# Kernel tuning notes

Hardware: AMD Instinct MI355X
Metric: run time of the kernel (lower is better)

Reference implementation:

```python
import jax, jax.numpy as jnp
import numpy as np

N = 100000
E = 1200000
D = 64
EPS = 1e-15
ATANH_CLIP = 1.0 - 1e-7


def _logmap0(x, c):
    # Poincare ball logmap at origin: artanh(sqrt(c)||x||) * x / (sqrt(c)||x||)
    sqrt_c = jnp.sqrt(c)
    norm = jnp.maximum(jnp.linalg.norm(x, axis=-1, keepdims=True), EPS)
    arg = jnp.minimum(sqrt_c * norm, ATANH_CLIP)
    return jnp.arctanh(arg) * x / (sqrt_c * norm)


def _expmap0(u, c):
    # Poincare ball expmap at origin: tanh(sqrt(c)||u||) * u / (sqrt(c)||u||)
    sqrt_c = jnp.sqrt(c)
    norm = jnp.maximum(jnp.linalg.norm(u, axis=-1, keepdims=True), EPS)
    return jnp.tanh(sqrt_c * norm) * u / (sqrt_c * norm)


def setup_inputs() -> dict:
    key = jax.random.key(0)
    ks = jax.random.split(key, 8)
    src = jax.random.randint(ks[0], (E,), 0, N)
    dst = jax.random.randint(ks[1], (E,), 0, N)
    # scale embeddings so points lie inside the unit Poincare ball
    emb = jax.random.normal(ks[2], (N, D), dtype=jnp.float32) * 0.01
    W1 = jax.random.normal(ks[3], (D, D), dtype=jnp.float32) * 0.05
    b1 = jax.random.normal(ks[4], (D,), dtype=jnp.float32) * 0.01
    W2 = jax.random.normal(ks[5], (D, D), dtype=jnp.float32) * 0.05
    b2 = jax.random.normal(ks[6], (D,), dtype=jnp.float32) * 0.01
    curvature = -jnp.ones((1,), dtype=jnp.float32)
    return {"src": src, "dst": dst, "emb": emb, "W1": W1, "b1": b1,
            "W2": W2, "b2": b2, "curvature": curvature}


def reference(src, dst, emb, W1, b1, W2, b2, curvature):
    c = jnp.abs(curvature)[0]
    # in-degree for DGL-style mean (zero-degree nodes get 0)
    deg = jax.ops.segment_sum(jnp.ones((E,), dtype=emb.dtype), dst, num_segments=N)
    inv_deg = jnp.where(deg > 0, 1.0 / jnp.maximum(deg, 1.0), 0.0)[:, None]

    x = emb
    for W, b in ((W1, b1), (W2, b2)):
        tangent = _logmap0(x, c)                         # [N, D]
        h = tangent @ W.T + b                            # [N, D]
        neigh = jax.ops.segment_sum(h[src], dst, num_segments=N) * inv_deg  # scatter-mean
        x = _expmap0(neigh, c)
    return x
```

## Files before the change

kernel.cpp:

```cpp
#include <hip/hip_runtime.h>
#include <math.h>

#define DIM 64
#define EPSF 1e-15f

#define BW_SHIFT 8
#define BW (1 << BW_SHIFT)
#define CAP_SHIFT 12
#define CAP (1 << CAP_SHIFT)

typedef __attribute__((ext_vector_type(8))) short short8;
typedef __attribute__((ext_vector_type(4))) float floatx4;
typedef __attribute__((ext_vector_type(2))) float floatx2;
typedef __attribute__((ext_vector_type(4))) unsigned int uintx4;

__device__ __forceinline__ float group16_sum(float x) {
#pragma unroll
    for (int off = 1; off <= 8; off <<= 1)
        x += __shfl_xor(x, off, 64);
    return x;
}
__device__ __forceinline__ float group8_sum(float x) {
#pragma unroll
    for (int off = 1; off <= 4; off <<= 1)
        x += __shfl_xor(x, off, 64);
    return x;
}
__device__ __forceinline__ unsigned int f2bf(float x) {
    unsigned int u = __float_as_uint(x);
    u += 0x7fffu + ((u >> 16) & 1u);
    return u >> 16;
}
__device__ __forceinline__ float bflo(unsigned int u) { return __uint_as_float(u << 16); }
__device__ __forceinline__ float bfhi(unsigned int u) { return __uint_as_float(u & 0xFFFF0000u); }

__global__ void prep_kernel(const float* __restrict__ W1, const float* __restrict__ W2,
                            unsigned short* __restrict__ Wbf1, unsigned short* __restrict__ Wbf2,
                            unsigned short* __restrict__ zrowb, int* __restrict__ cursorB, int NB) {
    int i = blockIdx.x * 256 + threadIdx.x;
    if (i < DIM * DIM) {
        Wbf1[i] = (unsigned short)f2bf(W1[i]);
        Wbf2[i] = (unsigned short)f2bf(W2[i]);
    }
    if (i < NB) cursorB[i] = i << CAP_SHIFT;
    if (blockIdx.x == 0 && threadIdx.x < 64) zrowb[threadIdx.x] = 0;
}

__global__ __launch_bounds__(256) void partition_kernel(
    const int* __restrict__ src, const int* __restrict__ dst,
    int* __restrict__ cursorB, unsigned int* __restrict__ pairBuf, int E, int NB)
{
    __shared__ int hist[512], gbase[512], lcur[512];
    int tid = threadIdx.x;
    for (int t = tid; t < NB; t += 256) { hist[t] = 0; lcur[t] = 0; }
    __syncthreads();
    int base = blockIdx.x * 4096;
    unsigned int packed[16]; int bkt[16];
#pragma unroll
    for (int i = 0; i < 16; ++i) {
        int e = base + i * 256 + tid;
        if (e < E) {
            int s = src[e], d = dst[e];
            bkt[i] = d >> BW_SHIFT;
            packed[i] = ((unsigned int)(d & (BW - 1)) << 17) | (unsigned int)s;
            atomicAdd(&hist[bkt[i]], 1);
        } else bkt[i] = -1;
    }
    __syncthreads();
    for (int t = tid; t < NB; t += 256)
        gbase[t] = hist[t] ? atomicAdd(&cursorB[t], hist[t]) : 0;
    __syncthreads();
#pragma unroll
    for (int i = 0; i < 16; ++i) {
        if (bkt[i] >= 0) {
            int rank = atomicAdd(&lcur[bkt[i]], 1);
            int p = gbase[bkt[i]] + rank;
            if (p < ((bkt[i] + 1) << CAP_SHIFT)) pairBuf[p] = packed[i];
        }
    }
}

union SharedU {
    struct {
        int edges[CAP];
        int stage[CAP];
        int hist[BW], cur[BW], tmp[BW];
    } s;
    unsigned int atile[4][16 * 36];
};

__global__ __launch_bounds__(256, 4) void sort_and_gemm_kernel(
    const unsigned int* __restrict__ pairBuf, const int* __restrict__ cursorB,
    int* __restrict__ rowS, int* __restrict__ rowE, int* __restrict__ col,
    const float* __restrict__ in, const unsigned short* __restrict__ Wbf,
    const float* __restrict__ bias, const float* __restrict__ curv,
    unsigned short* __restrict__ outb, int N, int NB)
{
    __shared__ SharedU u;
    if ((int)blockIdx.x < NB) {
        const int b = blockIdx.x, t = threadIdx.x;
        const int base = b << CAP_SHIFT;
        int cnt = cursorB[b] - base;
        if (cnt > CAP) cnt = CAP;
        for (int i = t; i < cnt; i += 256) u.s.edges[i] = (int)pairBuf[base + i];
        u.s.hist[t] = 0;
        __syncthreads();
        for (int i = t; i < cnt; i += 256) atomicAdd(&u.s.hist[u.s.edges[i] >> 17], 1);
        __syncthreads();
        int hv = u.s.hist[t];
        u.s.tmp[t] = hv; __syncthreads();
        for (int off = 1; off < 256; off <<= 1) {
            int x = (t >= off) ? u.s.tmp[t - off] : 0; __syncthreads();
            u.s.tmp[t] += x; __syncthreads();
        }
        int excl = u.s.tmp[t] - hv;
        int node = (b << BW_SHIFT) + t;
        if (node < N) { rowS[node] = base + excl; rowE[node] = base + excl + hv; }
        u.s.cur[t] = excl;
        __syncthreads();
        for (int i = t; i < cnt; i += 256) {
            int v = u.s.edges[i];
            int pos = atomicAdd(&u.s.cur[v >> 17], 1);
            u.s.stage[pos] = v & 0x1FFFF;
        }
        __syncthreads();
        for (int i = t; i < cnt; i += 256) col[base + i] = u.s.stage[i];
    } else {
        const int bid = blockIdx.x - NB;
        const int gemmWaves = (gridDim.x - NB) << 2;
        const float sc = sqrtf(fabsf(curv[0]));
        const float CLIPF = 1.0f - 1e-7f;
        const int lane = threadIdx.x & 63;
        const int wid  = threadIdx.x >> 6;
        const int q = lane >> 4, r = lane & 15;
        const int numBatches = (N + 15) >> 4;
        const float4* in4 = (const float4*)in;

        short8 bfrag[4][2];
#pragma unroll
        for (int nt = 0; nt < 4; ++nt)
#pragma unroll
            for (int ks = 0; ks < 2; ++ks)
                bfrag[nt][ks] = *(const short8*)(Wbf + (nt * 16 + r) * 64 + ks * 32 + q * 8);

        float biasv[4];
#pragma unroll
        for (int nt = 0; nt < 4; ++nt) biasv[nt] = bias[nt * 16 + r];

        for (int batch = (bid << 2) + wid; batch < numBatches; batch += gemmWaves) {
            const int base = batch << 4;
#pragma unroll
            for (int it = 0; it < 4; ++it) {
                int m = it * 4 + q;
                int node = base + m;
                float4 v = make_float4(0.f, 0.f, 0.f, 0.f);
                if (node < N) v = in4[(size_t)node * 16 + r];
                float ss = group16_sum(v.x * v.x + v.y * v.y + v.z * v.z + v.w * v.w);
                float nrm = fmaxf(sqrtf(ss), EPSF);
                float a = fminf(sc * nrm, CLIPF);
                float g = atanhf(a) / (sc * nrm);
                unsigned int lo = f2bf(v.x * g) | (f2bf(v.y * g) << 16);
                unsigned int hi = f2bf(v.z * g) | (f2bf(v.w * g) << 16);
                *(uint2*)&u.atile[wid][m * 36 + r * 2] = make_uint2(lo, hi);
            }
            floatx4 accm[4];
#pragma unroll
            for (int nt = 0; nt < 4; ++nt) accm[nt] = (floatx4){0.f, 0.f, 0.f, 0.f};
#pragma unroll
            for (int ks = 0; ks < 2; ++ks) {
                uintx4 ua = *(const uintx4*)&u.atile[wid][r * 36 + q * 4 + ks * 16];
                short8 af = __builtin_bit_cast(short8, ua);
#pragma unroll
                for (int nt = 0; nt < 4; ++nt)
                    accm[nt] = __builtin_amdgcn_mfma_f32_16x16x32_bf16(af, bfrag[nt][ks], accm[nt], 0, 0, 0);
            }
#pragma unroll
            for (int nt = 0; nt < 4; ++nt)
#pragma unroll
                for (int reg = 0; reg < 4; ++reg) {
                    int node = base + q * 4 + reg;
                    if (node < N)
                        outb[(size_t)node * 64 + nt * 16 + r] =
                            (unsigned short)f2bf(accm[nt][reg] + biasv[nt]);
                }
        }
    }
}

__device__ __forceinline__ void gather_rows_bf16(
    const char* __restrict__ hb, const int* __restrict__ col,
    int start, int end, int dmax, long long zoff, int g, int r, int colMax,
    floatx2 acc2[4])
{
    const int roff = r << 4;
    for (int b = 0; (b << 3) < dmax; ++b) {
        int pos = start + (b << 3) + r;
        int cv = col[min(pos, colMax)];
        int sent = (pos < end) ? cv : -1;
        int lim = dmax - (b << 3); if (lim > 8) lim = 8;
        if (lim == 8) {
            long long o[8];
#pragma unroll
            for (int i = 0; i < 8; ++i) {
                int s = __shfl(sent, (g << 3) + i, 64);
                o[i] = (s < 0) ? zoff : ((long long)s << 7);
            }
#pragma unroll
            for (int i = 0; i < 8; ++i) {
                uint4 uu = *(const uint4*)(hb + o[i] + roff);
                acc2[0] += (floatx2){bflo(uu.x), bfhi(uu.x)};
                acc2[1] += (floatx2){bflo(uu.y), bfhi(uu.y)};
                acc2[2] += (floatx2){bflo(uu.z), bfhi(uu.z)};
                acc2[3] += (floatx2){bflo(uu.w), bfhi(uu.w)};
            }
        } else {
            for (int i = 0; i < lim; ++i) {
                int s = __shfl(sent, (g << 3) + i, 64);
                long long o = (s < 0) ? zoff : ((long long)s << 7);
                uint4 uu = *(const uint4*)(hb + o + roff);
                acc2[0] += (floatx2){bflo(uu.x), bfhi(uu.x)};
                acc2[1] += (floatx2){bflo(uu.y), bfhi(uu.y)};
                acc2[2] += (floatx2){bflo(uu.z), bfhi(uu.z)};
                acc2[3] += (floatx2){bflo(uu.w), bfhi(uu.w)};
            }
        }
    }
}

__global__ __launch_bounds__(256, 4) void gather_gemm_mfma(
    const unsigned short* __restrict__ h, const int* __restrict__ rowS,
    const int* __restrict__ rowE, const int* __restrict__ col,
    const unsigned short* __restrict__ Wbf, const float* __restrict__ bias,
    unsigned short* __restrict__ outb, long long zoff, int N, int colMax)
{
    __shared__ unsigned int AtileU[4][16 * 36];
    const int lane = threadIdx.x & 63;
    const int wid  = threadIdx.x >> 6;
    const int q = lane >> 4, r = lane & 15;
    const int g8 = lane >> 3, r8 = lane & 7;
    const int wavesTotal = (gridDim.x * blockDim.x) >> 6;
    const int numBatches = (N + 15) >> 4;
    const char* hb = (const char*)h;

    short8 bfrag[4][2];
#pragma unroll
    for (int nt = 0; nt < 4; ++nt)
#pragma unroll
        for (int ks = 0; ks < 2; ++ks)
            bfrag[nt][ks] = *(const short8*)(Wbf + (nt * 16 + r) * 64 + ks * 32 + q * 8);

    float biasv[4];
#pragma unroll
    for (int nt = 0; nt < 4; ++nt) biasv[nt] = bias[nt * 16 + r];

    for (int batch = (blockIdx.x << 2) + wid; batch < numBatches; batch += wavesTotal) {
        const int base = batch << 4;
#pragma unroll
        for (int it = 0; it < 2; ++it) {
            int m = it * 8 + g8;
            int node = base + m;
            int start = 0, end = 0;
            if (node < N) { start = rowS[node]; end = rowE[node]; }
            int deg = end - start;
            int dmax = max(deg, __shfl_xor(deg, 8, 64));
            dmax = max(dmax, __shfl_xor(dmax, 16, 64));
            dmax = max(dmax, __shfl_xor(dmax, 32, 64));
            floatx2 acc2[4] = {{0.f,0.f},{0.f,0.f},{0.f,0.f},{0.f,0.f}};
            gather_rows_bf16(hb, col, start, end, dmax, zoff, g8, r8, colMax, acc2);
            float inv = (deg > 0) ? 1.f / (float)deg : 0.f;
            unsigned int u0 = f2bf(acc2[0].x * inv) | (f2bf(acc2[0].y * inv) << 16);
            unsigned int u1 = f2bf(acc2[1].x * inv) | (f2bf(acc2[1].y * inv) << 16);
            unsigned int u2 = f2bf(acc2[2].x * inv) | (f2bf(acc2[2].y * inv) << 16);
            unsigned int u3 = f2bf(acc2[3].x * inv) | (f2bf(acc2[3].y * inv) << 16);
            *(uint4*)&AtileU[wid][m * 36 + r8 * 4] = make_uint4(u0, u1, u2, u3);
        }
        floatx4 accm[4];
#pragma unroll
        for (int nt = 0; nt < 4; ++nt) accm[nt] = (floatx4){0.f, 0.f, 0.f, 0.f};
#pragma unroll
        for (int ks = 0; ks < 2; ++ks) {
            uintx4 ua = *(const uintx4*)&AtileU[wid][r * 36 + q * 4 + ks * 16];
            short8 af = __builtin_bit_cast(short8, ua);
#pragma unroll
            for (int nt = 0; nt < 4; ++nt)
                accm[nt] = __builtin_amdgcn_mfma_f32_16x16x32_bf16(af, bfrag[nt][ks], accm[nt], 0, 0, 0);
        }
#pragma unroll
        for (int nt = 0; nt < 4; ++nt)
#pragma unroll
            for (int reg = 0; reg < 4; ++reg) {
                int node = base + q * 4 + reg;
                if (node < N)
                    outb[(size_t)node * 64 + nt * 16 + r] =
                        (unsigned short)f2bf(accm[nt][reg] + biasv[nt]);
            }
    }
}

__global__ __launch_bounds__(256, 6) void gather_expmap8(
    const unsigned short* __restrict__ h, const int* __restrict__ rowS,
    const int* __restrict__ rowE, const int* __restrict__ col,
    const float* __restrict__ curv, float* __restrict__ out,
    long long zoff, int N, int colMax)
{
    const float sc = sqrtf(fabsf(curv[0]));
    const int lane = threadIdx.x & 63;
    const int wid  = threadIdx.x >> 6;
    const int g8 = lane >> 3, r8 = lane & 7;
    const int wavesTotal = (gridDim.x * blockDim.x) >> 6;
    const int numBatches = (N + 7) >> 3;
    const char* hb = (const char*)h;
    float4* out4 = (float4*)out;

    for (int batch = (blockIdx.x << 2) + wid; batch < numBatches; batch += wavesTotal) {
        int node = (batch << 3) + g8;
        int start = 0, end = 0;
        if (node < N) { start = rowS[node]; end = rowE[node]; }
        int deg = end - start;
        int dmax = max(deg, __shfl_xor(deg, 8, 64));
        dmax = max(dmax, __shfl_xor(dmax, 16, 64));
        dmax = max(dmax, __shfl_xor(dmax, 32, 64));
        floatx2 acc2[4] = {{0.f,0.f},{0.f,0.f},{0.f,0.f},{0.f,0.f}};
        gather_rows_bf16(hb, col, start, end, dmax, zoff, g8, r8, colMax, acc2);
        float inv = (deg > 0) ? 1.f / (float)deg : 0.f;
        float v[8], ss = 0.f;
#pragma unroll
        for (int j = 0; j < 4; ++j) {
            v[2*j]   = acc2[j].x * inv;
            v[2*j+1] = acc2[j].y * inv;
            ss += v[2*j] * v[2*j] + v[2*j+1] * v[2*j+1];
        }
        ss = group8_sum(ss);
        float nrm = fmaxf(sqrtf(ss), EPSF);
        float a = sc * nrm;
        float f = tanhf(a) / a;
        if (node < N) {
            out4[(size_t)node * 16 + r8 * 2]     = make_float4(v[0] * f, v[1] * f, v[2] * f, v[3] * f);
            out4[(size_t)node * 16 + r8 * 2 + 1] = make_float4(v[4] * f, v[5] * f, v[6] * f, v[7] * f);
        }
    }
}

extern "C" void kernel_launch(void* const* d_in, const int* in_sizes, int n_in,
                              void* d_out, int out_size, void* d_ws, size_t ws_size,
                              hipStream_t stream)
{
    const int*   src  = (const int*)d_in[0];
    const int*   dst  = (const int*)d_in[1];
    const float* emb  = (const float*)d_in[2];
    const float* W1   = (const float*)d_in[3];
    const float* b1   = (const float*)d_in[4];
    const float* W2   = (const float*)d_in[5];
    const float* b2   = (const float*)d_in[6];
    const float* curv = (const float*)d_in[7];
    float*       out  = (float*)d_out;

    const int E = in_sizes[0];
    const int N = in_sizes[2] / DIM;
    const int NB = (N + BW - 1) >> BW_SHIFT;
    const size_t bucketSlots = (size_t)NB << CAP_SHIFT;
    const int colMax = (int)bucketSlots - 1;

    char* ws = (char*)d_ws;
    auto align256 = [](size_t x) { return (x + 255) & ~(size_t)255; };
    size_t off = 0;
    int* cursorB            = (int*)(ws + off);            off += align256(512 * 4);
    int* rowS               = (int*)(ws + off);            off += align256((size_t)N * 4);
    int* rowE               = (int*)(ws + off);            off += align256((size_t)N * 4);
    unsigned int* pairBuf   = (unsigned int*)(ws + off);   off += align256(bucketSlots * 4);
    int* col                = (int*)(ws + off);            off += align256(bucketSlots * 4);
    unsigned short* Wbf1    = (unsigned short*)(ws + off); off += align256((size_t)DIM * DIM * 2);
    unsigned short* Wbf2    = (unsigned short*)(ws + off); off += align256((size_t)DIM * DIM * 2);
    unsigned short* zrowb   = (unsigned short*)(ws + off); off += align256(DIM * 2);
    unsigned short* h1b     = (unsigned short*)(ws + off); off += align256((size_t)N * DIM * 2);
    unsigned short* h2b     = (unsigned short*)(ws + off); off += align256((size_t)N * DIM * 2);

    const long long zoff_h1 = (long long)((char*)zrowb - (char*)h1b);
    const long long zoff_h2 = (long long)((char*)zrowb - (char*)h2b);

    const int chunkBlocks  = (E + 4095) / 4096;
    const int numBatches16 = (N + 15) / 16;
    const int blocks16     = (numBatches16 + 3) / 4;
    const int numBatches8  = (N + 7) / 8;
    const int blocks8      = (numBatches8 + 3) / 4;

    prep_kernel<<<(DIM * DIM + 255) / 256, 256, 0, stream>>>(W1, W2, Wbf1, Wbf2,
                                                             zrowb, cursorB, NB);
    partition_kernel<<<chunkBlocks, 256, 0, stream>>>(src, dst, cursorB, pairBuf, E, NB);
    sort_and_gemm_kernel<<<NB + blocks16, 256, 0, stream>>>(
        pairBuf, cursorB, rowS, rowE, col, emb, Wbf1, b1, curv, h1b, N, NB);
    gather_gemm_mfma<<<blocks16, 256, 0, stream>>>(h1b, rowS, rowE, col, Wbf2, b2, h2b,
                                                   zoff_h1, N, colMax);
    gather_expmap8<<<blocks8, 256, 0, stream>>>(h2b, rowS, rowE, col, curv, out,
                                                zoff_h2, N, colMax);
}
```

Before: 188.3 us.

## Route neighbor row gathers through global_load_lds DMA into shared staging buffers

Replaces the per-lane register gathers of bf16 neighbor rows with global_load_lds 16-byte DMA transfers into a per-wave LDS staging buffer, then reads the data back from LDS to accumulate. The aim is to cut VGPR pressure and issue overhead on the irregular gather. The trade-off is extra LDS traffic and full vmcnt and lgkmcnt waits on every 8-edge block, which serialise load and consume. The expmap kernel's launch-bounds occupancy hint drops from 6 to 4 to make room for the added 32 KB of LDS per block.

```diff
diff --git a/kernel.cpp b/kernel.cpp
--- a/kernel.cpp
+++ b/kernel.cpp
@@ -33,6 +33,14 @@
 }
 __device__ __forceinline__ float bflo(unsigned int u) { return __uint_as_float(u << 16); }
 __device__ __forceinline__ float bfhi(unsigned int u) { return __uint_as_float(u & 0xFFFF0000u); }
+
+__device__ __forceinline__ void dma16(const void* g, void* l) {
+    __builtin_amdgcn_global_load_lds(
+        (const __attribute__((address_space(1))) unsigned int*)g,
+        (__attribute__((address_space(3))) unsigned int*)l, 16, 0, 0);
+}
+#define WAIT_VM0()   __builtin_amdgcn_s_waitcnt(0x0F70)
+#define WAIT_LGKM0() __builtin_amdgcn_s_waitcnt(0xC07F)
 
 __global__ void prep_kernel(const float* __restrict__ W1, const float* __restrict__ W2,
                             unsigned short* __restrict__ Wbf1, unsigned short* __restrict__ Wbf2,
@@ -187,42 +195,33 @@
     }
 }
 
-__device__ __forceinline__ void gather_rows_bf16(
+__device__ __forceinline__ void gather_rows_dma(
     const char* __restrict__ hb, const int* __restrict__ col,
-    int start, int end, int dmax, long long zoff, int g, int r, int colMax,
-    floatx2 acc2[4])
+    int start, int end, int dmax, long long zoff, int g, int r, int lane,
+    int colMax, uint4* wbuf, floatx2 acc2[4])
 {
     const int roff = r << 4;
-    for (int b = 0; (b << 3) < dmax; ++b) {
-        int pos = start + (b << 3) + r;
+    const char* zptr = hb + zoff;
+    char* wb = (char*)wbuf;
+    for (int sblk = 0; sblk < dmax; sblk += 8) {
+        int pos = start + sblk + r;
         int cv = col[min(pos, colMax)];
         int sent = (pos < end) ? cv : -1;
-        int lim = dmax - (b << 3); if (lim > 8) lim = 8;
-        if (lim == 8) {
-            long long o[8];
-#pragma unroll
-            for (int i = 0; i < 8; ++i) {
-                int s = __shfl(sent, (g << 3) + i, 64);
-                o[i] = (s < 0) ? zoff : ((long long)s << 7);
-            }
-#pragma unroll
-            for (int i = 0; i < 8; ++i) {
-                uint4 uu = *(const uint4*)(hb + o[i] + roff);
-                acc2[0] += (floatx2){bflo(uu.x), bfhi(uu.x)};
-                acc2[1] += (floatx2){bflo(uu.y), bfhi(uu.y)};
-                acc2[2] += (floatx2){bflo(uu.z), bfhi(uu.z)};
-                acc2[3] += (floatx2){bflo(uu.w), bfhi(uu.w)};
-            }
-        } else {
-            for (int i = 0; i < lim; ++i) {
-                int s = __shfl(sent, (g << 3) + i, 64);
-                long long o = (s < 0) ? zoff : ((long long)s << 7);
-                uint4 uu = *(const uint4*)(hb + o + roff);
-                acc2[0] += (floatx2){bflo(uu.x), bfhi(uu.x)};
-                acc2[1] += (floatx2){bflo(uu.y), bfhi(uu.y)};
-                acc2[2] += (floatx2){bflo(uu.z), bfhi(uu.z)};
-                acc2[3] += (floatx2){bflo(uu.w), bfhi(uu.w)};
-            }
+        WAIT_LGKM0();
+#pragma unroll
+        for (int i = 0; i < 8; ++i) {
+            int s = __shfl(sent, (g << 3) + i, 64);
+            const char* gp = (s < 0) ? zptr : (hb + ((long long)s << 7));
+            dma16(gp + roff, (void*)(wb + i * 1024));
+        }
+        WAIT_VM0();
+#pragma unroll
+        for (int i = 0; i < 8; ++i) {
+            uint4 uu = *(const uint4*)(wb + i * 1024 + lane * 16);
+            acc2[0] += (floatx2){bflo(uu.x), bfhi(uu.x)};
+            acc2[1] += (floatx2){bflo(uu.y), bfhi(uu.y)};
+            acc2[2] += (floatx2){bflo(uu.z), bfhi(uu.z)};
+            acc2[3] += (floatx2){bflo(uu.w), bfhi(uu.w)};
         }
     }
 }
@@ -234,6 +233,7 @@
     unsigned short* __restrict__ outb, long long zoff, int N, int colMax)
 {
     __shared__ unsigned int AtileU[4][16 * 36];
+    __shared__ uint4 gbuf[4][512];
     const int lane = threadIdx.x & 63;
     const int wid  = threadIdx.x >> 6;
     const int q = lane >> 4, r = lane & 15;
@@ -241,6 +241,7 @@
     const int wavesTotal = (gridDim.x * blockDim.x) >> 6;
     const int numBatches = (N + 15) >> 4;
     const char* hb = (const char*)h;
+    uint4* wbuf = gbuf[wid];
 
     short8 bfrag[4][2];
 #pragma unroll
@@ -266,7 +267,7 @@
             dmax = max(dmax, __shfl_xor(dmax, 16, 64));
             dmax = max(dmax, __shfl_xor(dmax, 32, 64));
             floatx2 acc2[4] = {{0.f,0.f},{0.f,0.f},{0.f,0.f},{0.f,0.f}};
-            gather_rows_bf16(hb, col, start, end, dmax, zoff, g8, r8, colMax, acc2);
+            gather_rows_dma(hb, col, start, end, dmax, zoff, g8, r8, lane, colMax, wbuf, acc2);
             float inv = (deg > 0) ? 1.f / (float)deg : 0.f;
             unsigned int u0 = f2bf(acc2[0].x * inv) | (f2bf(acc2[0].y * inv) << 16);
             unsigned int u1 = f2bf(acc2[1].x * inv) | (f2bf(acc2[1].y * inv) << 16);
@@ -297,12 +298,13 @@
     }
 }
 
-__global__ __launch_bounds__(256, 6) void gather_expmap8(
+__global__ __launch_bounds__(256, 4) void gather_expmap8(
     const unsigned short* __restrict__ h, const int* __restrict__ rowS,
     const int* __restrict__ rowE, const int* __restrict__ col,
     const float* __restrict__ curv, float* __restrict__ out,
     long long zoff, int N, int colMax)
 {
+    __shared__ uint4 gbuf[4][512];
     const float sc = sqrtf(fabsf(curv[0]));
     const int lane = threadIdx.x & 63;
     const int wid  = threadIdx.x >> 6;
@@ -311,6 +313,7 @@
     const int numBatches = (N + 7) >> 3;
     const char* hb = (const char*)h;
     float4* out4 = (float4*)out;
+    uint4* wbuf = gbuf[wid];
 
     for (int batch = (blockIdx.x << 2) + wid; batch < numBatches; batch += wavesTotal) {
         int node = (batch << 3) + g8;
@@ -321,7 +324,7 @@
         dmax = max(dmax, __shfl_xor(dmax, 16, 64));
         dmax = max(dmax, __shfl_xor(dmax, 32, 64));
         floatx2 acc2[4] = {{0.f,0.f},{0.f,0.f},{0.f,0.f},{0.f,0.f}};
-        gather_rows_bf16(hb, col, start, end, dmax, zoff, g8, r8, colMax, acc2);
+        gather_rows_dma(hb, col, start, end, dmax, zoff, g8, r8, lane, colMax, wbuf, acc2);
         float inv = (deg > 0) ? 1.f / (float)deg : 0.f;
         float v[8], ss = 0.f;
 #pragma unroll
```

Result: slower. 192.9 us (+2.4%).
